# Kernel optimization log

Measured on AMD Instinct MI355X. Metric: run time of the kernel, lower is better.

## Reference

```python
import jax, jax.numpy as jnp
import numpy as np

EPS = 1e-5  # torch BatchNorm default


def setup_inputs() -> dict:
    key = jax.random.key(0)
    k1, k2, k3 = jax.random.split(key, 3)
    N, C, T, V, O = 64, 64, 300, 25, 64
    x = jax.random.normal(k1, (N, C, T, V), dtype=jnp.float32)
    # 24 = V-1 convs, each (O, C, 1, 2) -> packed as (V-1, O, C, 2), scaled like conv_init
    W = jax.random.normal(k2, (V - 1, O, C, 2), dtype=jnp.float32) * (1.0 / np.sqrt(2 * C))
    b = jax.random.normal(k3, (V - 1, O), dtype=jnp.float32) * 0.01
    gamma = jnp.ones((O,), dtype=jnp.float32)
    beta = jnp.zeros((O,), dtype=jnp.float32)
    return {"x": x, "W": W, "b": b, "gamma": gamma, "beta": beta}


def reference(x, W, b, gamma, beta):
    # x: (N, C, T, V); W: (V-1, O, C, 2); b: (V-1, O)
    # Math of the original loop: out[..., v] = sum_i W0_i @ x[..., v]
    #   + sum_i W1_i @ x[..., (v+i+1) % V] + sum_i b_i
    V = x.shape[-1]
    W0 = W[..., 0]  # (V-1, O, C)
    W1 = W[..., 1]  # (V-1, O, C)
    # identity-tap term: all W0 share the same column -> sum once
    S0 = W0.sum(axis=0)  # (O, C)
    out = jnp.einsum('oc,nctv->notv', S0, x)
    # circular term: source u = (v+i+1)%V  <=>  i = (u-v-1)%V, valid for u != v
    v_idx = jnp.arange(V)
    off = (v_idx[None, :] - v_idx[:, None] - 1) % V  # (V_target, V_source) -> i, equals V-1 when u==v
    W1p = jnp.concatenate([W1, jnp.zeros_like(W1[:1])], axis=0)  # index V-1 maps to zero (u==v excluded)
    Wg = W1p[off]  # (V, V, O, C), zero on the diagonal
    out = out + jnp.einsum('vuoc,nctu->notv', Wg, x)
    out = out + b.sum(axis=0)[None, :, None, None]
    # BatchNorm2d (training-mode batch stats, biased variance) + ReLU
    mean = out.mean(axis=(0, 2, 3), keepdims=True)
    var = out.var(axis=(0, 2, 3), keepdims=True)
    out = (out - mean) * jax.lax.rsqrt(var + EPS)
    out = out * gamma[None, :, None, None] + beta[None, :, None, None]
    return jax.nn.relu(out)
```

## Files before the change

kernel.cpp:

```cpp
#include <hip/hip_runtime.h>


typedef short  s16x8 __attribute__((ext_vector_type(8)));
typedef float  f32x4 __attribute__((ext_vector_type(4)));

#define T_      300
#define TB_     19
#define NTHR_   320
#define ASTR    144
#define TSTR    404

__device__ __forceinline__ unsigned short f2bf(float f) {
  unsigned u = __builtin_bit_cast(unsigned, f);
  return (unsigned short)((u + 0x7FFFu + ((u >> 16) & 1u)) >> 16);
}

__global__ void pack_w_kernel(const float* __restrict__ W, s16x8* __restrict__ Wg) {
  int idx = blockIdx.x * 256 + threadIdx.x;
  if (idx >= 12800) return;
  int lane  = idx & 63;
  int ni    = (idx >> 6) & 3;
  int chunk = (idx >> 8) & 1;
  int s     = idx >> 9;
  int o     = (ni << 4) + (lane & 15);
  int cbase = (chunk << 5) + ((lane >> 4) << 3);
  s16x8 h;
#pragma unroll
  for (int j = 0; j < 8; ++j) {
    int c = cbase + j;
    float val;
    if (s == 0) {
      val = 0.f;
      for (int i = 0; i < 24; ++i) val += W[((i * 64 + o) * 64 + c) * 2];
    } else {
      val = W[(((s - 1) * 64 + o) * 64 + c) * 2 + 1];
    }
    h[j] = (short)f2bf(val);
  }
  Wg[idx] = h;
}

#define MF(J, Q0, Q1, Q2, Q3, SR)                                               \
  acc[J][0] = __builtin_amdgcn_mfma_f32_16x16x32_bf16(SR, Q0, acc[J][0], 0, 0, 0); \
  acc[J][1] = __builtin_amdgcn_mfma_f32_16x16x32_bf16(SR, Q1, acc[J][1], 0, 0, 0); \
  acc[J][2] = __builtin_amdgcn_mfma_f32_16x16x32_bf16(SR, Q2, acc[J][2], 0, 0, 0); \
  acc[J][3] = __builtin_amdgcn_mfma_f32_16x16x32_bf16(SR, Q3, acc[J][3], 0, 0, 0);

#define ADV(J)                                                                  \
  { bool w_ = (u[J] == 24); u[J] = w_ ? 0 : u[J] + 1;                           \
    ao[J] += w_ ? -(24 * ASTR) : ASTR; }

#define PHASE(BA0, BA1, BA2, BA3, BA4, BA5, BA6, BA7, SN)                       \
  {                                                                             \
    const s16x8* wq_ = Wg + (SN) * 512;                                         \
    MF(0, BA0, BA1, BA2, BA3, S0) S0 = *(const s16x8*)(Ash + ao[0] + 64);       \
    MF(1, BA0, BA1, BA2, BA3, S1) S1 = *(const s16x8*)(Ash + ao[1] + 64);       \
    MF(2, BA0, BA1, BA2, BA3, S2) S2 = *(const s16x8*)(Ash + ao[2] + 64);       \
    MF(3, BA0, BA1, BA2, BA3, S3) S3 = *(const s16x8*)(Ash + ao[3] + 64);       \
    MF(4, BA0, BA1, BA2, BA3, S4) S4 = *(const s16x8*)(Ash + ao[4] + 64);       \
    BA0 = wq_[lane];       BA1 = wq_[64 + lane];                                \
    BA2 = wq_[128 + lane]; BA3 = wq_[192 + lane];                               \
    ADV(0) MF(0, BA4, BA5, BA6, BA7, S0) S0 = *(const s16x8*)(Ash + ao[0]);     \
    ADV(1) MF(1, BA4, BA5, BA6, BA7, S1) S1 = *(const s16x8*)(Ash + ao[1]);     \
    ADV(2) MF(2, BA4, BA5, BA6, BA7, S2) S2 = *(const s16x8*)(Ash + ao[2]);     \
    ADV(3) MF(3, BA4, BA5, BA6, BA7, S3) S3 = *(const s16x8*)(Ash + ao[3]);     \
    ADV(4) MF(4, BA4, BA5, BA6, BA7, S4) S4 = *(const s16x8*)(Ash + ao[4]);     \
    BA4 = wq_[256 + lane]; BA5 = wq_[320 + lane];                               \
    BA6 = wq_[384 + lane]; BA7 = wq_[448 + lane];                               \
  }

__global__ __launch_bounds__(NTHR_) void tap_mm_kernel(
    const float* __restrict__ x, const s16x8* __restrict__ Wg,
    float* __restrict__ out, float* __restrict__ partials) {
  __shared__ __align__(16) char Ash[57600];
  __shared__ float red2[640];
  int n  = blockIdx.x;
  int tb = blockIdx.y;
  int t0 = tb * 16;
  int validRows = min(16, T_ - t0) * 25;
  int tid = threadIdx.x;
  const float* xn = x + n * 480000 + t0 * 25;

  int wid = tid >> 6, lane = tid & 63;
  int l15 = lane & 15, lk = lane >> 4;

  s16x8 bfA0 = Wg[lane],       bfA1 = Wg[64 + lane];
  s16x8 bfA2 = Wg[128 + lane], bfA3 = Wg[192 + lane];
  s16x8 bfA4 = Wg[256 + lane], bfA5 = Wg[320 + lane];
  s16x8 bfA6 = Wg[384 + lane], bfA7 = Wg[448 + lane];
  s16x8 bfB0 = Wg[512 + lane], bfB1 = Wg[576 + lane];
  s16x8 bfB2 = Wg[640 + lane], bfB3 = Wg[704 + lane];
  s16x8 bfB4 = Wg[768 + lane], bfB5 = Wg[832 + lane];
  s16x8 bfB6 = Wg[896 + lane], bfB7 = Wg[960 + lane];

#pragma unroll 5
  for (int it = 0; it < 10; ++it) {
    int id  = tid + it * NTHR_;
    int pos = id % 400;
    int g   = id / 400;
    bool vld = pos < validRows;
    s16x8 h;
#pragma unroll
    for (int j = 0; j < 8; ++j) {
      float f = vld ? xn[((g << 3) + j) * 7500 + pos] : 0.f;
      h[j] = (short)f2bf(f);
    }
    *(s16x8*)(Ash + pos * ASTR + (g << 4)) = h;
  }

  int u[5], ao[5];
#pragma unroll
  for (int r = 0; r < 5; ++r) {
    int orow = ((wid * 5 + r) << 4) + l15;
    int tL = orow / 25;
    u[r]  = orow - tL * 25;
    ao[r] = orow * ASTR + (lk << 4);
  }
  f32x4 acc[5][4];
#pragma unroll
  for (int r = 0; r < 5; ++r)
#pragma unroll
    for (int ct = 0; ct < 4; ++ct) acc[r][ct] = (f32x4){0.f, 0.f, 0.f, 0.f};

  __syncthreads();

  s16x8 S0 = *(const s16x8*)(Ash + ao[0]);
  s16x8 S1 = *(const s16x8*)(Ash + ao[1]);
  s16x8 S2 = *(const s16x8*)(Ash + ao[2]);
  s16x8 S3 = *(const s16x8*)(Ash + ao[3]);
  s16x8 S4 = *(const s16x8*)(Ash + ao[4]);

  for (int k = 0; k < 12; ++k) {
    int sA = 2 * k + 2;
    int sB = 2 * k + 3; sB -= (sB >= 25) ? 25 : 0;
    PHASE(bfA0, bfA1, bfA2, bfA3, bfA4, bfA5, bfA6, bfA7, sA)
    PHASE(bfB0, bfB1, bfB2, bfB3, bfB4, bfB5, bfB6, bfB7, sB)
  }
  PHASE(bfA0, bfA1, bfA2, bfA3, bfA4, bfA5, bfA6, bfA7, 1)

  float s1v[4] = {0.f, 0.f, 0.f, 0.f}, s2v[4] = {0.f, 0.f, 0.f, 0.f};
#pragma unroll
  for (int r = 0; r < 5; ++r) {
#pragma unroll
    for (int qq = 0; qq < 4; ++qq) {
      int orow = ((wid * 5 + r) << 4) + (lk << 2) + qq;
      if (orow < validRows) {
#pragma unroll
        for (int ct = 0; ct < 4; ++ct) {
          float val = acc[r][ct][qq];
          s1v[ct] += val;
          s2v[ct] += val * val;
        }
      }
    }
  }
#pragma unroll
  for (int ct = 0; ct < 4; ++ct) {
    float a = s1v[ct], b = s2v[ct];
    a += __shfl_xor(a, 16); a += __shfl_xor(a, 32);
    b += __shfl_xor(b, 16); b += __shfl_xor(b, 32);
    if (lane < 16) {
      int base = ((((wid << 2) + ct) << 4) + l15) * 2;
      red2[base]     = a;
      red2[base + 1] = b;
    }
  }

  float* T = (float*)Ash;
  float* outb = out + n * 480000 + tb * 400;
  for (int qt = 0; qt < 4; ++qt) {
    __syncthreads();
#pragma unroll
    for (int r = 0; r < 5; ++r) {
      int row0 = wid * 80 + r * 16 + (lk << 2);
      *(f32x4*)&T[l15 * TSTR + row0] = acc[r][qt];
    }
    __syncthreads();
    if (qt == 0 && tid < 128) {
      int o = tid >> 1, m = tid & 1;
      int ct = o >> 4, ol = o & 15;
      float sres = 0.f;
#pragma unroll
      for (int w = 0; w < 5; ++w) sres += red2[((((w << 2) + ct) << 4) + ol) * 2 + m];
      int bl = blockIdx.y * 64 + blockIdx.x;
      partials[bl * 128 + m * 64 + o] = sres;
    }
#pragma unroll
    for (int i = 0; i < 5; ++i) {
      int idx = tid + i * 320;
      int ol  = idx / 100;
      int r4  = idx - ol * 100;
      if ((r4 << 2) < validRows) {
        float4 v = *(float4*)&T[ol * TSTR + (r4 << 2)];
        *(float4*)&outb[((qt << 4) + ol) * 7500 + (r4 << 2)] = v;
      }
    }
  }
}

__global__ void finalize_kernel(const float* __restrict__ part,
                                const float* __restrict__ gamma,
                                const float* __restrict__ beta,
                                float* __restrict__ scsh) {
  __shared__ float sm[512];
  int o = blockIdx.x;
  int tid = threadIdx.x;
  float s1 = 0.f, s2 = 0.f;
  for (int b = tid; b < 1216; b += 256) {
    s1 += part[b * 128 + o];
    s2 += part[b * 128 + 64 + o];
  }
  sm[tid] = s1; sm[256 + tid] = s2;
  __syncthreads();
  for (int st = 128; st >= 1; st >>= 1) {
    if (tid < st) { sm[tid] += sm[tid + st]; sm[256 + tid] += sm[256 + tid + st]; }
    __syncthreads();
  }
  if (tid == 0) {
    const float inv = 1.0f / 480000.0f;
    float mean = sm[0] * inv;
    float var  = sm[256] * inv - mean * mean;
    float sc = gamma[o] * rsqrtf(var + 1e-5f);
    float sh = beta[o] - mean * sc;
    scsh[o]      = sc;
    scsh[64 + o] = sh;
  }
}

__global__ void bn_relu_kernel(float4* __restrict__ out, const float* __restrict__ scsh) {
  int i = blockIdx.x * blockDim.x + threadIdx.x;
  const int total = 7680000;
  int stride = gridDim.x * blockDim.x;
  for (; i < total; i += stride) {
    int o = (i / 1875) & 63;
    float sc = scsh[o], sh = scsh[64 + o];
    float4 v = out[i];
    v.x = fmaxf(fmaf(v.x, sc, sh), 0.f);
    v.y = fmaxf(fmaf(v.y, sc, sh), 0.f);
    v.z = fmaxf(fmaf(v.z, sc, sh), 0.f);
    v.w = fmaxf(fmaf(v.w, sc, sh), 0.f);
    out[i] = v;
  }
}

extern "C" void kernel_launch(void* const* d_in, const int* in_sizes, int n_in,
                              void* d_out, int out_size, void* d_ws, size_t ws_size,
                              hipStream_t stream) {
  const float* x     = (const float*)d_in[0];
  const float* W     = (const float*)d_in[1];
  const float* gamma = (const float*)d_in[3];
  const float* beta  = (const float*)d_in[4];
  float* out = (float*)d_out;

  char* ws = (char*)d_ws;
  s16x8* Wg       = (s16x8*)ws;
  float* partials = (float*)(ws + 204800);
  float* scsh     = (float*)(ws + 204800 + 622592);

  pack_w_kernel<<<dim3(50), dim3(256), 0, stream>>>(W, Wg);
  tap_mm_kernel<<<dim3(64, TB_), dim3(NTHR_), 0, stream>>>(x, Wg, out, partials);
  finalize_kernel<<<dim3(64), dim3(256), 0, stream>>>(partials, gamma, beta, scsh);
  bn_relu_kernel<<<dim3(2048), dim3(256), 0, stream>>>((float4*)out, scsh);
}
```

Baseline: 208.0 us.

## Retile tap GEMM into flat 256-row tiles with 4 waves per block

Replaces the 16-timestep tiles (400 rows, 5 waves, 320 threads) with flat 256-row tiles over the T*V dimension, giving 30 blocks per sample and 256 threads per block. Each block stages a slab of up to 300 input rows spanning the timesteps its rows touch, and maps rows to slab offsets for the circular neighbor lookup. The smaller block and LDS footprint may raise occupancy and cut tail waste from the partial last time tile. In exchange the grid is larger, with more partial-stat blocks for finalize to reduce, and each tile loads some extra halo rows.

```diff
diff --git a/kernel.cpp b/kernel.cpp
--- a/kernel.cpp
+++ b/kernel.cpp
@@ -4,11 +4,12 @@
 typedef short  s16x8 __attribute__((ext_vector_type(8)));
 typedef float  f32x4 __attribute__((ext_vector_type(4)));
 
-#define T_      300
-#define TB_     19
-#define NTHR_   320
+#define NTHR_   256
+#define RPB_    256
+#define NBR_    30
+#define SLAB_   300
 #define ASTR    144
-#define TSTR    404
+#define TSTR    260
 
 __device__ __forceinline__ unsigned short f2bf(float f) {
   unsigned u = __builtin_bit_cast(unsigned, f);
@@ -57,14 +58,12 @@
     MF(1, BA0, BA1, BA2, BA3, S1) S1 = *(const s16x8*)(Ash + ao[1] + 64);       \
     MF(2, BA0, BA1, BA2, BA3, S2) S2 = *(const s16x8*)(Ash + ao[2] + 64);       \
     MF(3, BA0, BA1, BA2, BA3, S3) S3 = *(const s16x8*)(Ash + ao[3] + 64);       \
-    MF(4, BA0, BA1, BA2, BA3, S4) S4 = *(const s16x8*)(Ash + ao[4] + 64);       \
     BA0 = wq_[lane];       BA1 = wq_[64 + lane];                                \
     BA2 = wq_[128 + lane]; BA3 = wq_[192 + lane];                               \
     ADV(0) MF(0, BA4, BA5, BA6, BA7, S0) S0 = *(const s16x8*)(Ash + ao[0]);     \
     ADV(1) MF(1, BA4, BA5, BA6, BA7, S1) S1 = *(const s16x8*)(Ash + ao[1]);     \
     ADV(2) MF(2, BA4, BA5, BA6, BA7, S2) S2 = *(const s16x8*)(Ash + ao[2]);     \
     ADV(3) MF(3, BA4, BA5, BA6, BA7, S3) S3 = *(const s16x8*)(Ash + ao[3]);     \
-    ADV(4) MF(4, BA4, BA5, BA6, BA7, S4) S4 = *(const s16x8*)(Ash + ao[4]);     \
     BA4 = wq_[256 + lane]; BA5 = wq_[320 + lane];                               \
     BA6 = wq_[384 + lane]; BA7 = wq_[448 + lane];                               \
   }
@@ -72,15 +71,17 @@
 __global__ __launch_bounds__(NTHR_) void tap_mm_kernel(
     const float* __restrict__ x, const s16x8* __restrict__ Wg,
     float* __restrict__ out, float* __restrict__ partials) {
-  __shared__ __align__(16) char Ash[57600];
-  __shared__ float red2[640];
-  int n  = blockIdx.x;
-  int tb = blockIdx.y;
-  int t0 = tb * 16;
-  int validRows = min(16, T_ - t0) * 25;
+  __shared__ __align__(16) char Ash[SLAB_ * ASTR];
+  __shared__ float red2[512];
+  int br = blockIdx.x, n = blockIdx.y;
+  int r0 = br * RPB_;
+  int validR = min(RPB_, 7500 - r0);
+  int t0g = r0 / 25;
+  int tlast = (r0 + validR - 1) / 25;
+  int slabRows = (tlast - t0g + 1) * 25;
+  const float* xn = x + n * 480000;
+  int xbase = t0g * 25;
   int tid = threadIdx.x;
-  const float* xn = x + n * 480000 + t0 * 25;
-
   int wid = tid >> 6, lane = tid & 63;
   int l15 = lane & 15, lk = lane >> 4;
 
@@ -95,32 +96,33 @@
 
 #pragma unroll 5
   for (int it = 0; it < 10; ++it) {
-    int id  = tid + it * NTHR_;
-    int pos = id % 400;
-    int g   = id / 400;
-    bool vld = pos < validRows;
-    s16x8 h;
-#pragma unroll
-    for (int j = 0; j < 8; ++j) {
-      float f = vld ? xn[((g << 3) + j) * 7500 + pos] : 0.f;
-      h[j] = (short)f2bf(f);
-    }
-    *(s16x8*)(Ash + pos * ASTR + (g << 4)) = h;
-  }
-
-  int u[5], ao[5];
-#pragma unroll
-  for (int r = 0; r < 5; ++r) {
-    int orow = ((wid * 5 + r) << 4) + l15;
-    int tL = orow / 25;
-    u[r]  = orow - tL * 25;
-    ao[r] = orow * ASTR + (lk << 4);
-  }
-  f32x4 acc[5][4];
-#pragma unroll
-  for (int r = 0; r < 5; ++r)
-#pragma unroll
-    for (int ct = 0; ct < 4; ++ct) acc[r][ct] = (f32x4){0.f, 0.f, 0.f, 0.f};
+    int id = tid + it * NTHR_;
+    if (id < 2400) {
+      int g = id / 300, pos = id - g * 300;
+      bool vld = pos < slabRows;
+      s16x8 h;
+#pragma unroll
+      for (int j = 0; j < 8; ++j) {
+        float f = vld ? xn[((g << 3) + j) * 7500 + xbase + pos] : 0.f;
+        h[j] = (short)f2bf(f);
+      }
+      *(s16x8*)(Ash + pos * ASTR + (g << 4)) = h;
+    }
+  }
+
+  int u[4], ao[4];
+#pragma unroll
+  for (int rt = 0; rt < 4; ++rt) {
+    int gr = r0 + (wid << 6) + (rt << 4) + l15;
+    int tL = gr / 25;
+    u[rt]  = gr - tL * 25;
+    ao[rt] = ((tL - t0g) * 25 + u[rt]) * ASTR + (lk << 4);
+  }
+  f32x4 acc[4][4];
+#pragma unroll
+  for (int rt = 0; rt < 4; ++rt)
+#pragma unroll
+    for (int ct = 0; ct < 4; ++ct) acc[rt][ct] = (f32x4){0.f, 0.f, 0.f, 0.f};
 
   __syncthreads();
 
@@ -128,7 +130,6 @@
   s16x8 S1 = *(const s16x8*)(Ash + ao[1]);
   s16x8 S2 = *(const s16x8*)(Ash + ao[2]);
   s16x8 S3 = *(const s16x8*)(Ash + ao[3]);
-  s16x8 S4 = *(const s16x8*)(Ash + ao[4]);
 
   for (int k = 0; k < 12; ++k) {
     int sA = 2 * k + 2;
@@ -140,14 +141,14 @@
 
   float s1v[4] = {0.f, 0.f, 0.f, 0.f}, s2v[4] = {0.f, 0.f, 0.f, 0.f};
 #pragma unroll
-  for (int r = 0; r < 5; ++r) {
+  for (int rt = 0; rt < 4; ++rt) {
 #pragma unroll
     for (int qq = 0; qq < 4; ++qq) {
-      int orow = ((wid * 5 + r) << 4) + (lk << 2) + qq;
-      if (orow < validRows) {
+      int rloc = (wid << 6) + (rt << 4) + (lk << 2) + qq;
+      if (rloc < validR) {
 #pragma unroll
         for (int ct = 0; ct < 4; ++ct) {
-          float val = acc[r][ct][qq];
+          float val = acc[rt][ct][qq];
           s1v[ct] += val;
           s2v[ct] += val * val;
         }
@@ -167,13 +168,13 @@
   }
 
   float* T = (float*)Ash;
-  float* outb = out + n * 480000 + tb * 400;
+  float* outb = out + n * 480000 + r0;
   for (int qt = 0; qt < 4; ++qt) {
     __syncthreads();
 #pragma unroll
-    for (int r = 0; r < 5; ++r) {
-      int row0 = wid * 80 + r * 16 + (lk << 2);
-      *(f32x4*)&T[l15 * TSTR + row0] = acc[r][qt];
+    for (int rt = 0; rt < 4; ++rt) {
+      int row0 = (wid << 6) + (rt << 4) + (lk << 2);
+      *(f32x4*)&T[l15 * TSTR + row0] = acc[rt][qt];
     }
     __syncthreads();
     if (qt == 0 && tid < 128) {
@@ -181,16 +182,15 @@
       int ct = o >> 4, ol = o & 15;
       float sres = 0.f;
 #pragma unroll
-      for (int w = 0; w < 5; ++w) sres += red2[((((w << 2) + ct) << 4) + ol) * 2 + m];
-      int bl = blockIdx.y * 64 + blockIdx.x;
+      for (int w = 0; w < 4; ++w) sres += red2[((((w << 2) + ct) << 4) + ol) * 2 + m];
+      int bl = blockIdx.y * NBR_ + blockIdx.x;
       partials[bl * 128 + m * 64 + o] = sres;
     }
 #pragma unroll
-    for (int i = 0; i < 5; ++i) {
-      int idx = tid + i * 320;
-      int ol  = idx / 100;
-      int r4  = idx - ol * 100;
-      if ((r4 << 2) < validRows) {
+    for (int it = 0; it < 4; ++it) {
+      int idx = tid + it * NTHR_;
+      int ol = idx >> 6, r4 = idx & 63;
+      if ((r4 << 2) < validR) {
         float4 v = *(float4*)&T[ol * TSTR + (r4 << 2)];
         *(float4*)&outb[((qt << 4) + ol) * 7500 + (r4 << 2)] = v;
       }
@@ -206,7 +206,7 @@
   int o = blockIdx.x;
   int tid = threadIdx.x;
   float s1 = 0.f, s2 = 0.f;
-  for (int b = tid; b < 1216; b += 256) {
+  for (int b = tid; b < 1920; b += 256) {
     s1 += part[b * 128 + o];
     s2 += part[b * 128 + 64 + o];
   }
@@ -255,10 +255,10 @@
   char* ws = (char*)d_ws;
   s16x8* Wg       = (s16x8*)ws;
   float* partials = (float*)(ws + 204800);
-  float* scsh     = (float*)(ws + 204800 + 622592);
+  float* scsh     = (float*)(ws + 204800 + 983040);
 
   pack_w_kernel<<<dim3(50), dim3(256), 0, stream>>>(W, Wg);
-  tap_mm_kernel<<<dim3(64, TB_), dim3(NTHR_), 0, stream>>>(x, Wg, out, partials);
+  tap_mm_kernel<<<dim3(NBR_, 64), dim3(NTHR_), 0, stream>>>(x, Wg, out, partials);
   finalize_kernel<<<dim3(64), dim3(256), 0, stream>>>(partials, gamma, beta, scsh);
   bn_relu_kernel<<<dim3(2048), dim3(256), 0, stream>>>((float4*)out, scsh);
 }
```

After: 234.1 us. +12.5%, slower.
